# Performance work log

Measured on AMD Instinct MI355X. Metric: run time of the kernel, lower is better.

The kernel has to match this reference:

```python
import jax, jax.numpy as jnp
import numpy as np

N = 50000
SELF_LOOP_W = 2.0  # GCNConv(improved=True)


def gcn_conv(x, edge_index, W, b):
    # x: [N, Fin], edge_index: [2, E] (row=source, col=target)
    h = x @ W  # [N, Fout]
    row, col = edge_index[0], edge_index[1]
    ones = jnp.ones(row.shape[0], dtype=h.dtype)
    deg = jax.ops.segment_sum(ones, col, num_segments=N) + SELF_LOOP_W
    dinv = jnp.where(deg > 0, jax.lax.rsqrt(deg), 0.0)
    norm = dinv[row] * dinv[col]  # [E]
    agg = jax.ops.segment_sum(norm[:, None] * h[row], col, num_segments=N)
    # self-loop contribution: weight 2.0, norm = dinv[i]^2
    agg = agg + (SELF_LOOP_W * dinv * dinv)[:, None] * h
    return agg + b


def setup_inputs() -> dict:
    key = jax.random.key(0)
    ks = jax.random.split(key, 12)
    F_in, H1, H2, H3 = 256, 256, 128, 64
    E, Ep, En = 800000, 200000, 200000
    def glorot(k, shape):
        lim = np.sqrt(6.0 / (shape[0] + shape[1]))
        return jax.random.uniform(k, shape, jnp.float32, -lim, lim)
    return {
        "x": jax.random.normal(ks[0], (N, F_in), jnp.float32),
        "train_edge_index": jax.random.randint(ks[1], (2, E), 0, N),
        "pos_edge_index": jax.random.randint(ks[2], (2, Ep), 0, N),
        "neg_edge_index": jax.random.randint(ks[3], (2, En), 0, N),
        "W1": glorot(ks[4], (F_in, H1)),
        "b1": jnp.zeros((H1,), jnp.float32),
        "W2": glorot(ks[5], (H1, H2)),
        "b2": jnp.zeros((H2,), jnp.float32),
        "Wl1": glorot(ks[6], (H2, H3)),
        "bl1": jnp.zeros((H3,), jnp.float32),
        "Wl2": glorot(ks[7], (H3, 1)),
        "bl2": jnp.zeros((1,), jnp.float32),
    }


def reference(x, train_edge_index, pos_edge_index, neg_edge_index,
              W1, b1, W2, b2, Wl1, bl1, Wl2, bl2):
    h = jax.nn.relu(gcn_conv(x, train_edge_index, W1, b1))
    h = gcn_conv(h, train_edge_index, W2, b2)  # [N, 128]
    tei = jnp.concatenate([pos_edge_index, neg_edge_index], axis=-1)  # [2, Ep+En]
    e = h[tei[1]] + h[tei[0]]  # x_i + x_j, [Etot, 128]
    e = jax.nn.relu(e @ Wl1 + bl1)
    e = jax.nn.sigmoid(e @ Wl2 + bl2)
    return e.reshape(-1)
```

## Files before the change

kernel.cpp:

```cpp
#include <hip/hip_runtime.h>
#include <math.h>

#define NV 50000
#define ETR 800000
#define EPOS 200000
#define ETEST 400000

typedef __attribute__((ext_vector_type(8))) short bf16x8;
typedef __attribute__((ext_vector_type(8))) unsigned short ushortx8;
typedef __attribute__((ext_vector_type(4))) float f32x4;

__device__ inline unsigned short f2b(float f) {
    union { float f; unsigned u; } v; v.f = f;
    unsigned r = v.u + 0x7fffu + ((v.u >> 16) & 1u);
    return (unsigned short)(r >> 16);
}
__device__ inline float blo(unsigned q) { union { unsigned u; float f; } v; v.u = q << 16; return v.f; }
__device__ inline float bhi(unsigned q) { union { unsigned u; float f; } v; v.u = q & 0xffff0000u; return v.f; }
__device__ inline float b2f(unsigned short s) { union { unsigned u; float f; } v; v.u = ((unsigned)s) << 16; return v.f; }

__device__ inline ushortx8 bf16add8(ushortx8 a, ushortx8 b) {
    ushortx8 r;
    #pragma unroll
    for (int i = 0; i < 8; ++i)
        r[i] = f2b(b2f(a[i]) + b2f(b[i]));
    return r;
}


template<int N, int K, bool AF32>
__device__ __forceinline__ void gemm_body(
    const void* __restrict__ Av, const unsigned short* __restrict__ Bt,
    unsigned short* __restrict__ C, int M, int row0, int col0)
{
    constexpr int BK = 64;
    __shared__ unsigned short Asm[128][BK];
    __shared__ unsigned short Bsm[128][BK];
    int tid = threadIdx.x;
    int lane = tid & 63, wid = tid >> 6;
    int wr = wid >> 1, wc = wid & 1;

    int sr = tid >> 3;
    int s8 = tid & 7;
    int sswz = s8 ^ (sr & 7);
    int fr = lane & 15;
    int g  = lane >> 4;

    f32x4 acc[4][4] = {};

    for (int k0 = 0; k0 < K; k0 += BK) {
        #pragma unroll
        for (int i = 0; i < 4; ++i) {
            int r = sr + i * 32;
            int gr = row0 + r;
            ushortx8 va = {0, 0, 0, 0, 0, 0, 0, 0};
            if constexpr (AF32) {
                const float* Af = (const float*)Av;
                if (gr < M) {
                    float4 f0 = *(const float4*)&Af[(size_t)gr * K + k0 + s8 * 8];
                    float4 f1 = *(const float4*)&Af[(size_t)gr * K + k0 + s8 * 8 + 4];
                    va[0] = f2b(f0.x); va[1] = f2b(f0.y); va[2] = f2b(f0.z); va[3] = f2b(f0.w);
                    va[4] = f2b(f1.x); va[5] = f2b(f1.y); va[6] = f2b(f1.z); va[7] = f2b(f1.w);
                }
            } else {
                const unsigned short* Ab = (const unsigned short*)Av;
                if (gr < M) va = *(const ushortx8*)&Ab[(size_t)gr * K + k0 + s8 * 8];
            }
            *(ushortx8*)&Asm[r][sswz * 8] = va;
            ushortx8 vb = *(const ushortx8*)&Bt[(size_t)(col0 + r) * K + k0 + s8 * 8];
            *(ushortx8*)&Bsm[r][sswz * 8] = vb;
        }
        __syncthreads();
        #pragma unroll
        for (int kf = 0; kf < BK; kf += 32) {
            int sbase = kf >> 3;
            bf16x8 af[4], bfr[4];
            #pragma unroll
            for (int m = 0; m < 4; ++m) {
                int rr = wr * 64 + m * 16 + fr;
                af[m] = *(const bf16x8*)&Asm[rr][((sbase + g) ^ (fr & 7)) * 8];
            }
            #pragma unroll
            for (int n = 0; n < 4; ++n) {
                int rr = wc * 64 + n * 16 + fr;
                bfr[n] = *(const bf16x8*)&Bsm[rr][((sbase + g) ^ (fr & 7)) * 8];
            }
            #pragma unroll
            for (int m = 0; m < 4; ++m)
                #pragma unroll
                for (int n = 0; n < 4; ++n)
                    acc[m][n] = __builtin_amdgcn_mfma_f32_16x16x32_bf16(af[m], bfr[n], acc[m][n], 0, 0, 0);
        }
        __syncthreads();
    }

    #pragma unroll
    for (int m = 0; m < 4; ++m) {
        int rbase = row0 + wr * 64 + m * 16 + g * 4;
        #pragma unroll
        for (int j = 0; j < 4; ++j) {
            int r = rbase + j;
            if (r < M) {
                #pragma unroll
                for (int n = 0; n < 4; ++n) {
                    int c = col0 + wc * 64 + n * 16 + fr;
                    C[(size_t)r * N + c] = f2b(acc[m][n][j]);
                }
            }
        }
    }
}


__global__ __launch_bounds__(256) void fat0_kernel(
    const int* __restrict__ tei, int* __restrict__ deg,
    const float* __restrict__ W1, unsigned short* __restrict__ w1t)
{
    int bid = blockIdx.x;
    int t = threadIdx.x;
    if (bid < 3125) {
        int e = bid * 256 + t;
        if (e < ETR) atomicAdd(&deg[tei[ETR + e]], 1);
    } else {
        int i = (bid - 3125) * 256 + t;
        int n = i >> 8, k = i & 255;
        w1t[i] = f2b(W1[k * 256 + n]);
    }
}


__global__ __launch_bounds__(256) void fat1_kernel(
    const float* __restrict__ x, const unsigned short* __restrict__ w1t,
    unsigned short* __restrict__ h1lin,
    const int* __restrict__ deg, int* __restrict__ partials,
    const float* __restrict__ W2, unsigned short* __restrict__ w2t,
    const float* __restrict__ Wl1, unsigned short* __restrict__ wl1t)
{
    int bid = blockIdx.x;
    int t = threadIdx.x;
    if (bid < 782) {
        int row0 = (bid >> 1) * 128, col0 = (bid & 1) * 128;
        gemm_body<256, 256, true>(x, w1t, h1lin, NV, row0, col0);
    } else if (bid < 831) {
        int p = bid - 782;
        int base = p * 1024;
        int s = 0;
        #pragma unroll
        for (int k = 0; k < 4; ++k) {
            int i = base + t + k * 256;
            if (i < NV) s += deg[i];
        }
        #pragma unroll
        for (int off = 32; off > 0; off >>= 1) s += __shfl_xor(s, off);
        __shared__ int ws4[4];
        if ((t & 63) == 0) ws4[t >> 6] = s;
        __syncthreads();
        if (t == 0) partials[p] = ws4[0] + ws4[1] + ws4[2] + ws4[3];
    } else if (bid < 959) {
        int i = (bid - 831) * 256 + t;
        int n = i >> 8, k = i & 255;
        w2t[i] = f2b(W2[k * 128 + n]);
    } else {
        int i = (bid - 959) * 256 + t;
        int n = i >> 7, k = i & 127;
        wl1t[i] = f2b(Wl1[k * 64 + n]);
    }
}


__global__ __launch_bounds__(1024) void ptr_kernel(
    const int* __restrict__ deg, const int* __restrict__ partials,
    int* __restrict__ ptr, int* __restrict__ cursor, float* __restrict__ dinv)
{
    int b = blockIdx.x, t = threadIdx.x;
    int i = b * 1024 + t;
    int d = (i < NV) ? deg[i] : 0;
    int lane = t & 63, w = t >> 6;
    int v = d;
    #pragma unroll
    for (int off = 1; off < 64; off <<= 1) {
        int u = __shfl_up(v, off);
        if (lane >= off) v += u;
    }
    __shared__ int wsum[16], woff[16];
    if (lane == 63) wsum[w] = v;
    __syncthreads();
    if (t == 0) {
        int s = 0;
        for (int k = 0; k < b; ++k) s += partials[k];
        for (int k = 0; k < 16; ++k) { woff[k] = s; s += wsum[k]; }
    }
    __syncthreads();
    int excl = woff[w] + v - d;
    if (i < NV) {
        ptr[i] = excl;
        cursor[i] = excl;
        dinv[i] = rsqrtf((float)d + 2.0f);
        if (i == NV - 1) ptr[NV] = excl + d;
    }
}

__global__ void fill_kernel(const int* __restrict__ tei, const float* __restrict__ dinv,
                            int* __restrict__ cursor, int2* __restrict__ edat) {
    int e = blockIdx.x * blockDim.x + threadIdx.x;
    if (e < ETR) {
        int row = tei[e];
        int col = tei[ETR + e];
        int p = atomicAdd(&cursor[col], 1);
        edat[p] = make_int2(row, __float_as_int(dinv[row] * dinv[col]));
    }
}


__global__ __launch_bounds__(256) void gemm2_kernel(
    const unsigned short* __restrict__ A, const unsigned short* __restrict__ Bt,
    unsigned short* __restrict__ C, int M)
{
    gemm_body<128, 256, false>(A, Bt, C, M, blockIdx.x * 128, 0);
}


template<int F, bool RELU>
__global__ __launch_bounds__(256) void gather_kernel(
    const int* __restrict__ ptr, const int2* __restrict__ edat,
    const float* __restrict__ dinv, const unsigned short* __restrict__ hlin,
    const float* __restrict__ bias, unsigned short* __restrict__ hout)
{
    constexpr int V = F / 64;
    int gid = blockIdx.x * blockDim.x + threadIdx.x;
    int node = gid >> 6, lane = gid & 63;
    if (node >= NV) return;
    float dc = dinv[node];
    int j0 = ptr[node], j1 = ptr[node + 1];
    float acc[V] = {};
    const unsigned short* hb = hlin + lane * V;
    const long long* edl = (const long long*)edat;

    int j = j0;
    for (; j + 7 < j1; j += 8) {
        long long e[8];
        #pragma unroll
        for (int u = 0; u < 8; ++u) e[u] = __builtin_nontemporal_load(edl + j + u);
        if constexpr (V == 4) {
            uint2 q[8];
            #pragma unroll
            for (int u = 0; u < 8; ++u)
                q[u] = *(const uint2*)(hb + (size_t)(int)e[u] * F);
            #pragma unroll
            for (int u = 0; u < 8; ++u) {
                float n = __int_as_float((int)(e[u] >> 32));
                acc[0] += n * blo(q[u].x);
                acc[1] += n * bhi(q[u].x);
                acc[2] += n * blo(q[u].y);
                acc[3] += n * bhi(q[u].y);
            }
        } else {
            unsigned q[8];
            #pragma unroll
            for (int u = 0; u < 8; ++u)
                q[u] = *(const unsigned*)(hb + (size_t)(int)e[u] * F);
            #pragma unroll
            for (int u = 0; u < 8; ++u) {
                float n = __int_as_float((int)(e[u] >> 32));
                acc[0] += n * blo(q[u]);
                acc[1] += n * bhi(q[u]);
            }
        }
    }
    for (; j + 3 < j1; j += 4) {
        long long e[4];
        #pragma unroll
        for (int u = 0; u < 4; ++u) e[u] = __builtin_nontemporal_load(edl + j + u);
        if constexpr (V == 4) {
            uint2 q[4];
            #pragma unroll
            for (int u = 0; u < 4; ++u)
                q[u] = *(const uint2*)(hb + (size_t)(int)e[u] * F);
            #pragma unroll
            for (int u = 0; u < 4; ++u) {
                float n = __int_as_float((int)(e[u] >> 32));
                acc[0] += n * blo(q[u].x);
                acc[1] += n * bhi(q[u].x);
                acc[2] += n * blo(q[u].y);
                acc[3] += n * bhi(q[u].y);
            }
        } else {
            unsigned q[4];
            #pragma unroll
            for (int u = 0; u < 4; ++u)
                q[u] = *(const unsigned*)(hb + (size_t)(int)e[u] * F);
            #pragma unroll
            for (int u = 0; u < 4; ++u) {
                float n = __int_as_float((int)(e[u] >> 32));
                acc[0] += n * blo(q[u]);
                acc[1] += n * bhi(q[u]);
            }
        }
    }
    for (; j < j1; ++j) {
        long long e0 = __builtin_nontemporal_load(edl + j);
        float n0 = __int_as_float((int)(e0 >> 32));
        if constexpr (V == 4) {
            uint2 q0 = *(const uint2*)(hb + (size_t)(int)e0 * F);
            acc[0] += n0 * blo(q0.x);
            acc[1] += n0 * bhi(q0.x);
            acc[2] += n0 * blo(q0.y);
            acc[3] += n0 * bhi(q0.y);
        } else {
            unsigned q0 = *(const unsigned*)(hb + (size_t)(int)e0 * F);
            acc[0] += n0 * blo(q0);
            acc[1] += n0 * bhi(q0);
        }
    }

    const unsigned short* ps = hb + (size_t)node * F;
    float sw = 2.0f * dc * dc;
    if constexpr (V == 4) {
        uint2 qs = *(const uint2*)ps;
        float o0 = acc[0] + sw * blo(qs.x) + bias[lane * 4 + 0];
        float o1 = acc[1] + sw * bhi(qs.x) + bias[lane * 4 + 1];
        float o2 = acc[2] + sw * blo(qs.y) + bias[lane * 4 + 2];
        float o3 = acc[3] + sw * bhi(qs.y) + bias[lane * 4 + 3];
        if (RELU) {
            o0 = fmaxf(o0, 0.f); o1 = fmaxf(o1, 0.f);
            o2 = fmaxf(o2, 0.f); o3 = fmaxf(o3, 0.f);
        }
        union { unsigned short u[4]; unsigned long long ll; } pk;
        pk.u[0] = f2b(o0); pk.u[1] = f2b(o1); pk.u[2] = f2b(o2); pk.u[3] = f2b(o3);
        __builtin_nontemporal_store(pk.ll, (unsigned long long*)(hout + (size_t)node * F + lane * 4));
    } else {
        unsigned qs = *(const unsigned*)ps;
        float o0 = acc[0] + sw * blo(qs) + bias[lane * 2 + 0];
        float o1 = acc[1] + sw * bhi(qs) + bias[lane * 2 + 1];
        if (RELU) { o0 = fmaxf(o0, 0.f); o1 = fmaxf(o1, 0.f); }
        union { unsigned short u[2]; unsigned q; } pk;
        pk.u[0] = f2b(o0); pk.u[1] = f2b(o1);
        __builtin_nontemporal_store(pk.q, (unsigned*)(hout + (size_t)node * F + lane * 2));
    }
}


__global__ __launch_bounds__(256) void edge_mlp_mfma_kernel(
    const int* __restrict__ pos, const int* __restrict__ neg,
    const unsigned short* __restrict__ h2, const unsigned short* __restrict__ Wl1t,
    const float* __restrict__ bl1, const float* __restrict__ Wl2,
    const float* __restrict__ bl2, float* __restrict__ out)
{
    __shared__ unsigned short Es[128][128];
    __shared__ unsigned short Ws[64][128];
    int tid = threadIdx.x;
    int lane = tid & 63, w = tid >> 6;
    int fr = lane & 15, g = lane >> 4;
    int e0 = blockIdx.x * 128;

    #pragma unroll
    for (int k = 0; k < 4; ++k) {
        int chunk = tid + k * 256;
        int row = chunk >> 4, c = chunk & 15;
        *(ushortx8*)&Ws[row][(c ^ (row & 7)) * 8] = *(const ushortx8*)&Wl1t[chunk * 8];
    }

    int et = tid >> 1, hh = tid & 1;
    int eg = e0 + et;
    int a, b;
    if (eg < EPOS) { a = pos[eg]; b = pos[EPOS + eg]; }
    else { int i = eg - EPOS; a = neg[i]; b = neg[EPOS + i]; }
    const unsigned short* pa = h2 + (size_t)a * 128 + hh * 64;
    const unsigned short* pb = h2 + (size_t)b * 128 + hh * 64;
    #pragma unroll
    for (int c8 = 0; c8 < 8; ++c8) {
        ushortx8 va = *(const ushortx8*)&pa[c8 * 8];
        ushortx8 vb = *(const ushortx8*)&pb[c8 * 8];
        ushortx8 vs = bf16add8(va, vb);
        int c = hh * 8 + c8;
        *(ushortx8*)&Es[et][(c ^ (et & 7)) * 8] = vs;
    }
    __syncthreads();

    f32x4 acc[2][4] = {};
    #pragma unroll
    for (int ks = 0; ks < 4; ++ks) {
        int c = ks * 4 + g;
        bf16x8 af[2], bfr[4];
        #pragma unroll
        for (int m = 0; m < 2; ++m) {
            int r = w * 32 + m * 16 + fr;
            af[m] = *(const bf16x8*)&Es[r][(c ^ (r & 7)) * 8];
        }
        #pragma unroll
        for (int n = 0; n < 4; ++n) {
            int r = n * 16 + fr;
            bfr[n] = *(const bf16x8*)&Ws[r][(c ^ (r & 7)) * 8];
        }
        #pragma unroll
        for (int m = 0; m < 2; ++m)
            #pragma unroll
            for (int n = 0; n < 4; ++n)
                acc[m][n] = __builtin_amdgcn_mfma_f32_16x16x32_bf16(af[m], bfr[n], acc[m][n], 0, 0, 0);
    }

    float bl2v = bl2[0];
    float b1v[4], w2v[4];
    #pragma unroll
    for (int n = 0; n < 4; ++n) {
        b1v[n] = bl1[n * 16 + fr];
        w2v[n] = Wl2[n * 16 + fr];
    }
    #pragma unroll
    for (int m = 0; m < 2; ++m) {
        float p[4];
        #pragma unroll
        for (int j = 0; j < 4; ++j) {
            float s = 0.f;
            #pragma unroll
            for (int n = 0; n < 4; ++n)
                s += fmaxf(acc[m][n][j] + b1v[n], 0.0f) * w2v[n];
            p[j] = s;
        }
        #pragma unroll
        for (int off = 1; off < 16; off <<= 1) {
            #pragma unroll
            for (int j = 0; j < 4; ++j)
                p[j] += __shfl_xor(p[j], off);
        }
        int ebase = e0 + w * 32 + m * 16 + g * 4;
        #pragma unroll
        for (int j = 0; j < 4; ++j)
            if (fr == j)
                out[ebase + j] = 1.0f / (1.0f + expf(-(p[j] + bl2v)));
    }
}


extern "C" void kernel_launch(void* const* d_in, const int* in_sizes, int n_in,
                              void* d_out, int out_size, void* d_ws, size_t ws_size,
                              hipStream_t stream) {
    const float* x   = (const float*)d_in[0];
    const int*   tei = (const int*)d_in[1];
    const int*   pos = (const int*)d_in[2];
    const int*   neg = (const int*)d_in[3];
    const float* W1  = (const float*)d_in[4];
    const float* b1  = (const float*)d_in[5];
    const float* W2  = (const float*)d_in[6];
    const float* b2  = (const float*)d_in[7];
    const float* Wl1 = (const float*)d_in[8];
    const float* bl1 = (const float*)d_in[9];
    const float* Wl2 = (const float*)d_in[10];
    const float* bl2 = (const float*)d_in[11];
    float* out = (float*)d_out;

    float* fws = (float*)d_ws;
    int*   iws = (int*)d_ws;
    unsigned short* usws = (unsigned short*)d_ws;
    float* dinv     = fws;
    int*   deg      = iws + 50000;
    int*   ptr      = iws + 100000;
    int*   cursor   = iws + 150002;
    int2*  edat     = (int2*)(iws + 200064);
    int*   partials = iws + 1800064;
    unsigned short* w1t  = usws + 2ull * 1800192;
    unsigned short* w2t  = usws + 2ull * 1832960;
    unsigned short* wl1t = usws + 2ull * 1849344;
    unsigned short* bufX = usws + 2ull * 1853504;
    unsigned short* bufL16 = usws + 2ull * 8253504;
    unsigned short* bufH = usws + 2ull * 14653504;

    hipMemsetAsync(deg, 0, NV * sizeof(int), stream);

    fat0_kernel<<<3381, 256, 0, stream>>>(tei, deg, W1, w1t);

    fat1_kernel<<<991, 256, 0, stream>>>(x, w1t, bufL16, deg, partials, W2, w2t, Wl1, wl1t);

    ptr_kernel<<<49, 1024, 0, stream>>>(deg, partials, ptr, cursor, dinv);
    fill_kernel<<<(ETR + 255) / 256, 256, 0, stream>>>(tei, dinv, cursor, edat);

    gather_kernel<256, true><<<(NV * 64) / 256, 256, 0, stream>>>(ptr, edat, dinv, bufL16, b1, bufH);

    gemm2_kernel<<<391, 256, 0, stream>>>(bufH, w2t, bufX, NV);
    gather_kernel<128, false><<<(NV * 64) / 256, 256, 0, stream>>>(ptr, edat, dinv, bufX, b2, bufL16);

    edge_mlp_mfma_kernel<<<ETEST / 128, 256, 0, stream>>>(pos, neg, bufL16, wl1t, bl1, Wl2, bl2, out);
}
```

Before: 291.7 us.

## Bucket test edges by source node to improve gather locality in edge MLP

Test edges are counting-sorted by their first endpoint, using a histogram, prefix scan and atomic fill added to the existing CSR-building kernels. The edge MLP then reads edges in sorted order and scatters results back through a permutation array. The aim is that consecutive edges share the h2 row of their source node, which improves cache reuse for that half of the gather. In exchange it adds atomics, extra index traffic and scattered output writes.

```diff
diff --git a/kernel.cpp b/kernel.cpp
--- a/kernel.cpp
+++ b/kernel.cpp
@@ -113,7 +113,8 @@
 
 
 __global__ __launch_bounds__(256) void fat0_kernel(
-    const int* __restrict__ tei, int* __restrict__ deg,
+    const int* __restrict__ tei, const int* __restrict__ pos, const int* __restrict__ neg,
+    int* __restrict__ deg, int* __restrict__ tdeg,
     const float* __restrict__ W1, unsigned short* __restrict__ w1t)
 {
     int bid = blockIdx.x;
@@ -121,10 +122,15 @@
     if (bid < 3125) {
         int e = bid * 256 + t;
         if (e < ETR) atomicAdd(&deg[tei[ETR + e]], 1);
+    } else if (bid < 4688) {
+        int e = (bid - 3125) * 256 + t;
+        if (e < ETEST) {
+            int a = (e < EPOS) ? pos[e] : neg[e - EPOS];
+            atomicAdd(&tdeg[a], 1);
+        }
     } else {
-        int i = (bid - 3125) * 256 + t;
-        int n = i >> 8, k = i & 255;
-        w1t[i] = f2b(W1[k * 256 + n]);
+        int i = (bid - 4688) * 256 + t;
+        w1t[i] = f2b(W1[(i & 255) * 256 + (i >> 8)]);
     }
 }
 
@@ -133,6 +139,7 @@
     const float* __restrict__ x, const unsigned short* __restrict__ w1t,
     unsigned short* __restrict__ h1lin,
     const int* __restrict__ deg, int* __restrict__ partials,
+    const int* __restrict__ tdeg, int* __restrict__ tpartials,
     const float* __restrict__ W2, unsigned short* __restrict__ w2t,
     const float* __restrict__ Wl1, unsigned short* __restrict__ wl1t)
 {
@@ -141,82 +148,110 @@
     if (bid < 782) {
         int row0 = (bid >> 1) * 128, col0 = (bid & 1) * 128;
         gemm_body<256, 256, true>(x, w1t, h1lin, NV, row0, col0);
-    } else if (bid < 831) {
-        int p = bid - 782;
+    } else if (bid < 880) {
+        int p = (bid - 782) % 49;
+        const int* src = (bid < 831) ? deg : tdeg;
+        int* dst = (bid < 831) ? partials : tpartials;
         int base = p * 1024;
         int s = 0;
         #pragma unroll
         for (int k = 0; k < 4; ++k) {
             int i = base + t + k * 256;
-            if (i < NV) s += deg[i];
+            if (i < NV) s += src[i];
         }
         #pragma unroll
         for (int off = 32; off > 0; off >>= 1) s += __shfl_xor(s, off);
         __shared__ int ws4[4];
         if ((t & 63) == 0) ws4[t >> 6] = s;
         __syncthreads();
-        if (t == 0) partials[p] = ws4[0] + ws4[1] + ws4[2] + ws4[3];
-    } else if (bid < 959) {
-        int i = (bid - 831) * 256 + t;
-        int n = i >> 8, k = i & 255;
-        w2t[i] = f2b(W2[k * 128 + n]);
+        if (t == 0) dst[p] = ws4[0] + ws4[1] + ws4[2] + ws4[3];
+    } else if (bid < 1008) {
+        int i = (bid - 880) * 256 + t;
+        w2t[i] = f2b(W2[(i & 255) * 128 + (i >> 8)]);
     } else {
-        int i = (bid - 959) * 256 + t;
-        int n = i >> 7, k = i & 127;
-        wl1t[i] = f2b(Wl1[k * 64 + n]);
+        int i = (bid - 1008) * 256 + t;
+        wl1t[i] = f2b(Wl1[(i & 127) * 64 + (i >> 7)]);
     }
 }
 
 
 __global__ __launch_bounds__(1024) void ptr_kernel(
     const int* __restrict__ deg, const int* __restrict__ partials,
-    int* __restrict__ ptr, int* __restrict__ cursor, float* __restrict__ dinv)
+    const int* __restrict__ tdeg, const int* __restrict__ tpartials,
+    int* __restrict__ ptr, int* __restrict__ cursor,
+    int* __restrict__ tcursor, float* __restrict__ dinv)
 {
     int b = blockIdx.x, t = threadIdx.x;
     int i = b * 1024 + t;
     int d = (i < NV) ? deg[i] : 0;
+    int td = (i < NV) ? tdeg[i] : 0;
     int lane = t & 63, w = t >> 6;
-    int v = d;
+    int v = d, tv = td;
     #pragma unroll
     for (int off = 1; off < 64; off <<= 1) {
         int u = __shfl_up(v, off);
-        if (lane >= off) v += u;
-    }
-    __shared__ int wsum[16], woff[16];
-    if (lane == 63) wsum[w] = v;
+        int tu = __shfl_up(tv, off);
+        if (lane >= off) { v += u; tv += tu; }
+    }
+    __shared__ int wsum[16], woff[16], twsum[16], twoff[16];
+    if (lane == 63) { wsum[w] = v; twsum[w] = tv; }
     __syncthreads();
     if (t == 0) {
-        int s = 0;
-        for (int k = 0; k < b; ++k) s += partials[k];
-        for (int k = 0; k < 16; ++k) { woff[k] = s; s += wsum[k]; }
+        int s = 0, ts = 0;
+        for (int k = 0; k < b; ++k) { s += partials[k]; ts += tpartials[k]; }
+        for (int k = 0; k < 16; ++k) {
+            woff[k] = s;  s += wsum[k];
+            twoff[k] = ts; ts += twsum[k];
+        }
     }
     __syncthreads();
     int excl = woff[w] + v - d;
+    int texcl = twoff[w] + tv - td;
     if (i < NV) {
         ptr[i] = excl;
         cursor[i] = excl;
+        tcursor[i] = texcl;
         dinv[i] = rsqrtf((float)d + 2.0f);
         if (i == NV - 1) ptr[NV] = excl + d;
     }
 }
 
-__global__ void fill_kernel(const int* __restrict__ tei, const float* __restrict__ dinv,
-                            int* __restrict__ cursor, int2* __restrict__ edat) {
-    int e = blockIdx.x * blockDim.x + threadIdx.x;
-    if (e < ETR) {
-        int row = tei[e];
-        int col = tei[ETR + e];
-        int p = atomicAdd(&cursor[col], 1);
-        edat[p] = make_int2(row, __float_as_int(dinv[row] * dinv[col]));
+
+__global__ void fill_kernel(const int* __restrict__ tei,
+                            const int* __restrict__ pos, const int* __restrict__ neg,
+                            const float* __restrict__ dinv,
+                            int* __restrict__ cursor, int2* __restrict__ edat,
+                            int* __restrict__ tcursor, int2* __restrict__ eab,
+                            int* __restrict__ eorig) {
+    int bid = blockIdx.x;
+    int t = threadIdx.x;
+    if (bid < 3125) {
+        int e = bid * 256 + t;
+        if (e < ETR) {
+            int row = tei[e];
+            int col = tei[ETR + e];
+            int p = atomicAdd(&cursor[col], 1);
+            edat[p] = make_int2(row, __float_as_int(dinv[row] * dinv[col]));
+        }
+    } else {
+        int e = (bid - 3125) * 256 + t;
+        if (e < ETEST) {
+            int a, b;
+            if (e < EPOS) { a = pos[e]; b = pos[EPOS + e]; }
+            else { int i = e - EPOS; a = neg[i]; b = neg[EPOS + i]; }
+            int p = atomicAdd(&tcursor[a], 1);
+            eab[p] = make_int2(a, b);
+            eorig[p] = e;
+        }
     }
 }
 
 
 __global__ __launch_bounds__(256) void gemm2_kernel(
     const unsigned short* __restrict__ A, const unsigned short* __restrict__ Bt,
-    unsigned short* __restrict__ C, int M)
-{
-    gemm_body<128, 256, false>(A, Bt, C, M, blockIdx.x * 128, 0);
+    unsigned short* __restrict__ C)
+{
+    gemm_body<128, 256, false>(A, Bt, C, NV, blockIdx.x * 128, 0);
 }
 
 
@@ -341,7 +376,7 @@
 
 
 __global__ __launch_bounds__(256) void edge_mlp_mfma_kernel(
-    const int* __restrict__ pos, const int* __restrict__ neg,
+    const int2* __restrict__ eab, const int* __restrict__ eorig,
     const unsigned short* __restrict__ h2, const unsigned short* __restrict__ Wl1t,
     const float* __restrict__ bl1, const float* __restrict__ Wl2,
     const float* __restrict__ bl2, float* __restrict__ out)
@@ -361,12 +396,9 @@
     }
 
     int et = tid >> 1, hh = tid & 1;
-    int eg = e0 + et;
-    int a, b;
-    if (eg < EPOS) { a = pos[eg]; b = pos[EPOS + eg]; }
-    else { int i = eg - EPOS; a = neg[i]; b = neg[EPOS + i]; }
-    const unsigned short* pa = h2 + (size_t)a * 128 + hh * 64;
-    const unsigned short* pb = h2 + (size_t)b * 128 + hh * 64;
+    int2 ab = eab[e0 + et];
+    const unsigned short* pa = h2 + (size_t)ab.x * 128 + hh * 64;
+    const unsigned short* pb = h2 + (size_t)ab.y * 128 + hh * 64;
     #pragma unroll
     for (int c8 = 0; c8 < 8; ++c8) {
         ushortx8 va = *(const ushortx8*)&pa[c8 * 8];
@@ -427,7 +459,7 @@
         #pragma unroll
         for (int j = 0; j < 4; ++j)
             if (fr == j)
-                out[ebase + j] = 1.0f / (1.0f + expf(-(p[j] + bl2v)));
+                out[eorig[ebase + j]] = 1.0f / (1.0f + expf(-(p[j] + bl2v)));
     }
 }
 
@@ -452,32 +484,38 @@
     float* fws = (float*)d_ws;
     int*   iws = (int*)d_ws;
     unsigned short* usws = (unsigned short*)d_ws;
-    float* dinv     = fws;
-    int*   deg      = iws + 50000;
-    int*   ptr      = iws + 100000;
-    int*   cursor   = iws + 150002;
-    int2*  edat     = (int2*)(iws + 200064);
-    int*   partials = iws + 1800064;
-    unsigned short* w1t  = usws + 2ull * 1800192;
-    unsigned short* w2t  = usws + 2ull * 1832960;
-    unsigned short* wl1t = usws + 2ull * 1849344;
-    unsigned short* bufX = usws + 2ull * 1853504;
-    unsigned short* bufL16 = usws + 2ull * 8253504;
-    unsigned short* bufH = usws + 2ull * 14653504;
-
-    hipMemsetAsync(deg, 0, NV * sizeof(int), stream);
-
-    fat0_kernel<<<3381, 256, 0, stream>>>(tei, deg, W1, w1t);
-
-    fat1_kernel<<<991, 256, 0, stream>>>(x, w1t, bufL16, deg, partials, W2, w2t, Wl1, wl1t);
-
-    ptr_kernel<<<49, 1024, 0, stream>>>(deg, partials, ptr, cursor, dinv);
-    fill_kernel<<<(ETR + 255) / 256, 256, 0, stream>>>(tei, dinv, cursor, edat);
+    float* dinv      = fws;
+    int*   deg       = iws + 50000;
+    int*   tdeg      = iws + 100000;
+    int*   ptr       = iws + 150064;
+    int*   cursor    = iws + 200128;
+    int*   tcursor   = iws + 250128;
+    int*   partials  = iws + 300160;
+    int*   tpartials = iws + 300224;
+    int2*  edat      = (int2*)(iws + 300288);
+    int2*  eab       = (int2*)(iws + 1900288);
+    int*   eorig     = iws + 2700288;
+    unsigned short* w1t  = usws + 2ull * 3100288;
+    unsigned short* w2t  = usws + 2ull * 3133056;
+    unsigned short* wl1t = usws + 2ull * 3149440;
+    unsigned short* bufX   = usws + 2ull * 3153536;
+    unsigned short* bufL16 = usws + 2ull * 6353536;
+    unsigned short* bufH   = usws + 2ull * 12753536;
+
+    hipMemsetAsync(deg, 0, 100000 * sizeof(int), stream);
+
+    fat0_kernel<<<4944, 256, 0, stream>>>(tei, pos, neg, deg, tdeg, W1, w1t);
+
+    fat1_kernel<<<1040, 256, 0, stream>>>(x, w1t, bufL16, deg, partials, tdeg, tpartials,
+                                          W2, w2t, Wl1, wl1t);
+
+    ptr_kernel<<<49, 1024, 0, stream>>>(deg, partials, tdeg, tpartials, ptr, cursor, tcursor, dinv);
+    fill_kernel<<<4688, 256, 0, stream>>>(tei, pos, neg, dinv, cursor, edat, tcursor, eab, eorig);
 
     gather_kernel<256, true><<<(NV * 64) / 256, 256, 0, stream>>>(ptr, edat, dinv, bufL16, b1, bufH);
 
-    gemm2_kernel<<<391, 256, 0, stream>>>(bufH, w2t, bufX, NV);
+    gemm2_kernel<<<391, 256, 0, stream>>>(bufH, w2t, bufX);
     gather_kernel<128, false><<<(NV * 64) / 256, 256, 0, stream>>>(ptr, edat, dinv, bufX, b2, bufL16);
 
-    edge_mlp_mfma_kernel<<<ETEST / 128, 256, 0, stream>>>(pos, neg, bufL16, wl1t, bl1, Wl2, bl2, out);
-}
+    edge_mlp_mfma_kernel<<<ETEST / 128, 256, 0, stream>>>(eab, eorig, bufL16, wl1t, bl1, Wl2, bl2, out);
+}
```

Measured after the change: 326.9 us. +12.1%, slower.
